# Optimization experiments

Measured on AMD Instinct MI355X. Metric: run time of the kernel, lower is better.

The kernel has to match this reference:

```python
import math
import jax, jax.numpy as jnp
import numpy as np

B = 2
TMAX = 1024
D = 1024
H = 16
DK = D // H
F = 4096
L = 2
CHUNK = 128
LEFT = 128
RIGHT = 32
EPS = 1e-5


def _build_mask(t_max, chunk, left, right):
    """Replicates EmformerEncoder.create_mask with audio_lens == t_max.
    Returns bool [T, T] where True = masked (disallowed), T = total_right + t_max."""
    num_chunks = math.ceil(t_max / chunk)
    ub = (num_chunks - 1) * right
    body = np.zeros((t_max, t_max), np.float32)
    mleft = np.zeros((t_max, ub), np.float32)
    mdiag = np.zeros((ub, ub), np.float32)
    mright = np.zeros((ub, t_max), np.float32)
    right_indexes = []
    for i in range(num_chunks):
        left_off = max(chunk * i - left, 0)
        start = chunk * i
        end = min(chunk * (i + 1), t_max)
        body[start:end, left_off:end] = 1
        if i == num_chunks - 1:
            break
        rem = t_max - (end + right)
        trl = right if rem >= 0 else t_max - end
        ri = len(right_indexes)
        mleft[start:start + chunk, ri:ri + trl] = 1
        mdiag[ri:ri + trl, ri:ri + trl] = 1
        mright[ri:ri + trl, left_off:end] = 1
        right_indexes += list(range(end, end + trl))
    rs = len(right_indexes)
    mleft = mleft[:, :rs]
    mdiag = mdiag[:rs, :rs]
    mright = mright[:rs, :]
    top = np.concatenate([mdiag, mright], axis=-1)
    bot = np.concatenate([mleft, body], axis=-1)
    m = np.concatenate([top, bot], axis=0)
    return m == 0  # True where attention is NOT allowed


def setup_inputs() -> dict:
    key = jax.random.key(0)
    ks = jax.random.split(key, 8)
    mask2d = _build_mask(TMAX, CHUNK, LEFT, RIGHT)  # [T, T]
    T = mask2d.shape[0]  # 1248
    w = lambda k, shape: jax.random.normal(k, shape, jnp.float32) * 0.02
    inp = {
        "input": jax.random.normal(ks[0], (B, T, D), jnp.float32),
        "ln_in_scale": jnp.ones((L, D), jnp.float32),
        "ln_in_bias": jnp.zeros((L, D), jnp.float32),
        "Wq": w(ks[1], (L, D, D)), "bq": jnp.zeros((L, D), jnp.float32),
        "Wk": w(ks[2], (L, D, D)), "bk": jnp.zeros((L, D), jnp.float32),
        "Wv": w(ks[3], (L, D, D)), "bv": jnp.zeros((L, D), jnp.float32),
        "ln1_scale": jnp.ones((L, D), jnp.float32),
        "ln1_bias": jnp.zeros((L, D), jnp.float32),
        "W1": w(ks[4], (L, D, F)), "b1": jnp.zeros((L, F), jnp.float32),
        "W2": w(ks[5], (L, F, D)), "b2": jnp.zeros((L, D), jnp.float32),
        "ln2_scale": jnp.ones((L, D), jnp.float32),
        "ln2_bias": jnp.zeros((L, D), jnp.float32),
        "mask": jnp.asarray(np.broadcast_to(mask2d[None, None], (B, 1, T, T)).copy()),
    }
    return inp


def _ln(x, scale, bias):
    m = jnp.mean(x, axis=-1, keepdims=True)
    v = jnp.mean(jnp.square(x - m), axis=-1, keepdims=True)
    return (x - m) * jax.lax.rsqrt(v + EPS) * scale + bias


def reference(input, ln_in_scale, ln_in_bias, Wq, bq, Wk, bk, Wv, bv,
              ln1_scale, ln1_bias, W1, b1, W2, b2, ln2_scale, ln2_bias, mask):
    x = input
    Bx, T, _ = x.shape
    scale = 1.0 / math.sqrt(DK)
    for l in range(L):
        h = _ln(x, ln_in_scale[l], ln_in_bias[l])  # pre-LN input (also residual base)
        q = (h @ Wq[l] + bq[l]).reshape(Bx, T, H, DK)
        k = (h @ Wk[l] + bk[l]).reshape(Bx, T, H, DK)
        v = (h @ Wv[l] + bv[l]).reshape(Bx, T, H, DK)
        scores = jnp.einsum('bqhd,bkhd->bhqk', q, k) * scale  # [B,H,T,T]
        scores = jnp.where(mask, -jnp.inf, scores)
        probs = jax.nn.softmax(scores, axis=-1)
        probs = jnp.where(mask, 0.0, probs)  # dropout_attn=0 -> identity
        o = jnp.einsum('bhqk,bkhd->bqhd', probs, v).reshape(Bx, T, D)
        attn_out = o + h
        y = _ln(attn_out, ln1_scale[l], ln1_bias[l])
        y = y @ W1[l] + b1[l]          # note: no activation in original code
        y = y @ W2[l] + b2[l] + attn_out
        x = _ln(y, ln2_scale[l], ln2_bias[l])
    return x
```

## Files before the change

### kernel.cpp

```cpp
#include <hip/hip_runtime.h>
#include <stdint.h>

typedef __attribute__((ext_vector_type(8))) short short8;
typedef __attribute__((ext_vector_type(4))) float f32x4;

#define DEV __device__ __forceinline__

DEV float bits2f(uint32_t u){ union{uint32_t u;float f;}v; v.u=u; return v.f; }
DEV float bf1(uint16_t s){ return bits2f(((uint32_t)s)<<16); }
DEV uint16_t f2bf(float f){ union{float f;uint32_t u;}v; v.f=f; uint32_t u=v.u;
  return (uint16_t)((u + 0x7fffu + ((u>>16)&1u))>>16); }
DEV uint16_t f2h(float a){ union{_Float16 h; uint16_t u;}v; v.h=(_Float16)a; return v.u; }
DEV float h2f(uint16_t s){ union{uint16_t u; _Float16 h;}v; v.u=s; return (float)v.h; }

DEV float ldval(const float* p, size_t i){ return p[i]; }
DEV float ldval(const uint16_t* p, size_t i){ return bf1(p[i]); }
DEV void stval(float* p, size_t i, float v){ p[i]=v; }
DEV void stval(uint16_t* p, size_t i, float v){ p[i]=f2bf(v); }

DEV void async16(const void* g, void* l){
#if __has_builtin(__builtin_amdgcn_global_load_lds)
  __builtin_amdgcn_global_load_lds((const __attribute__((address_space(1))) void*)g,
                                   (__attribute__((address_space(3))) void*)l, 16, 0, 0);
#else
  int lane = threadIdx.x & 63;
  *(uint4*)((char*)l + lane*16) = *(const uint4*)((const char*)g);
#endif
}

template<int TM, int TN, bool SPLIT>
__global__ __launch_bounds__(256) void gemm_t(
    const uint16_t* __restrict__ A, const uint16_t* __restrict__ Bt,
    const float* __restrict__ bias, void* __restrict__ Cout,
    int N, int K, int kchunk, ulong4 zofs) {
  __shared__ uint16_t sA[3][TM*32];
  __shared__ uint16_t sB[3][TN*32];
  constexpr int LPS = TM/64 + TN/64;
  const int lin = blockIdx.y*gridDim.x + blockIdx.x;
  const int q8 = (gridDim.x*gridDim.y) >> 3;
  const int swz = (lin & 7)*q8 + (lin >> 3);
  const int mt_ = swz % gridDim.y, nt_ = swz / gridDim.y;
  const int m0 = mt_*TM, n0 = nt_*TN;
  const int kb = SPLIT ? blockIdx.z*kchunk : 0;
  const int kend = SPLIT ? ((kb+kchunk < K) ? kb+kchunk : K) : K;
  const int tid = threadIdx.x, wid = tid>>6, lane = tid&63;
  constexpr int WM = TM/2, MT = WM/16;
  constexpr int WN = TN/2, NT = WN/16;
  const int wm = (wid&1)*WM, wn = (wid>>1)*WN;
  f32x4 acc[MT][NT];
  #pragma unroll
  for (int a=0;a<MT;a++)
    #pragma unroll
    for (int b=0;b<NT;b++) acc[a][b] = (f32x4){0.f,0.f,0.f,0.f};
  const int lrow = lane>>2;
  const int lcol = (((lane&3) ^ ((lrow>>1)&3)))*8;
  const int fr = lane&15, fc = lane>>4;
  const int rsw = (fc ^ ((fr>>1)&3))*8;

  auto stage = [&](int buf, int k0) {
    #pragma unroll
    for (int j = 0; j < TM/64; ++j) {
      int r0 = wid*(TM/4) + j*16;
      async16(A + (size_t)(m0+r0+lrow)*K + k0 + lcol, &sA[buf][r0*32]);
    }
    #pragma unroll
    for (int j = 0; j < TN/64; ++j) {
      int r0 = wid*(TN/4) + j*16;
      async16(Bt + (size_t)(n0+r0+lrow)*K + k0 + lcol, &sB[buf][r0*32]);
    }
  };

  const int niter = (kend - kb) >> 5;
  stage(0, kb);
  if (niter > 1) stage(1, kb + 32);
  int cur = 0;
  for (int it = 0; it < niter; ++it) {
    if (it+1 < niter) {
      if constexpr (LPS == 4)      asm volatile("s_waitcnt vmcnt(4)" ::: "memory");
      else if constexpr (LPS == 3) asm volatile("s_waitcnt vmcnt(3)" ::: "memory");
      else                         asm volatile("s_waitcnt vmcnt(2)" ::: "memory");
    } else {
      asm volatile("s_waitcnt vmcnt(0)" ::: "memory");
    }
    __builtin_amdgcn_s_barrier();
    __builtin_amdgcn_sched_barrier(0);
    if (it+2 < niter) {
      int b2 = cur+2; if (b2>=3) b2-=3;
      stage(b2, kb + (it+2)*32);
    }
    short8 af[MT], bfv[NT];
    #pragma unroll
    for (int t=0;t<MT;t++) af[t] = *(const short8*)&sA[cur][(wm + t*16 + fr)*32 + rsw];
    #pragma unroll
    for (int t=0;t<NT;t++) bfv[t] = *(const short8*)&sB[cur][(wn + t*16 + fr)*32 + rsw];
    #pragma unroll
    for (int mt=0;mt<MT;mt++)
      #pragma unroll
      for (int nt=0;nt<NT;nt++)
        acc[mt][nt] = __builtin_amdgcn_mfma_f32_16x16x32_bf16(af[mt], bfv[nt], acc[mt][nt], 0,0,0);
    if (++cur == 3) cur = 0;
  }
  const int cl = lane&15, rl = (lane>>4)*4;
  if (SPLIT) {
    size_t zo = (blockIdx.z==0) ? zofs.x : (blockIdx.z==1) ? zofs.y : zofs.z;
    float* Pz = (float*)((char*)Cout + zo);
    #pragma unroll
    for (int nt=0;nt<NT;nt++) {
      int n = n0 + wn + nt*16 + cl;
      #pragma unroll
      for (int mt=0;mt<MT;mt++)
        #pragma unroll
        for (int r=0;r<4;r++)
          Pz[(size_t)(m0 + wm + mt*16 + rl + r)*N + n] = acc[mt][nt][r];
    }
  } else {
    uint16_t* C = (uint16_t*)Cout;
    #pragma unroll
    for (int nt=0;nt<NT;nt++) {
      int n = n0 + wn + nt*16 + cl;
      float bv = bias ? bias[n] : 0.f;
      #pragma unroll
      for (int mt=0;mt<MT;mt++)
        #pragma unroll
        for (int r=0;r<4;r++)
          C[(size_t)(m0 + wm + mt*16 + rl + r)*N + n] = f2bf(acc[mt][nt][r] + bv);
    }
  }
}

template<typename TI, typename TO>
DEV void ln_body(int row, int tid, const TI* x, const float* sc, const float* bi,
                 TO* out, float* red) {
  const size_t base = (size_t)row*1024 + tid*4;
  float v0=ldval(x,base), v1=ldval(x,base+1), v2=ldval(x,base+2), v3=ldval(x,base+3);
  float s = v0+v1+v2+v3;
  float sq = v0*v0+v1*v1+v2*v2+v3*v3;
  #pragma unroll
  for (int off=32; off; off>>=1){ s += __shfl_xor(s,off); sq += __shfl_xor(sq,off); }
  int wid=tid>>6, lane=tid&63;
  if (lane==0){ red[wid]=s; red[4+wid]=sq; }
  __syncthreads();
  s = red[0]+red[1]+red[2]+red[3]; sq = red[4]+red[5]+red[6]+red[7];
  float mean = s*(1.f/1024.f);
  float inv  = rsqrtf(sq*(1.f/1024.f) - mean*mean + 1e-5f);
  int c = tid*4;
  stval(out, base,   (v0-mean)*inv*sc[c]   + bi[c]);
  stval(out, base+1, (v1-mean)*inv*sc[c+1] + bi[c+1]);
  stval(out, base+2, (v2-mean)*inv*sc[c+2] + bi[c+2]);
  stval(out, base+3, (v3-mean)*inv*sc[c+3] + bi[c+3]);
}

template<typename TI, typename TO>
__global__ __launch_bounds__(256) void ln_k(const TI* __restrict__ x,
    const float* __restrict__ sc, const float* __restrict__ bi,
    TO* __restrict__ out) {
  __shared__ float red[8];
  ln_body<TI,TO>(blockIdx.x, threadIdx.x, x, sc, bi, out, red);
}

template<typename TO>
__global__ __launch_bounds__(256) void ln2_fused(const char* __restrict__ wsb,
    const float* __restrict__ b2, const uint16_t* __restrict__ resid,
    const float* __restrict__ sc, const float* __restrict__ bi,
    TO* __restrict__ out) {
  const int row = blockIdx.x, tid = threadIdx.x;
  const size_t base = (size_t)row*1024 + tid*4;
  const float* P0 = (const float*)(wsb + 54538240);
  const float* P1 = (const float*)(wsb + 65024000);
  const float* P2 = (const float*)(wsb + 0);
  float4 p0 = *(const float4*)(P0 + base);
  float4 p1 = *(const float4*)(P1 + base);
  float4 p2 = *(const float4*)(P2 + base);
  int c = tid*4;
  float v0 = p0.x+p1.x+p2.x+b2[c]  +bf1(resid[base]);
  float v1 = p0.y+p1.y+p2.y+b2[c+1]+bf1(resid[base+1]);
  float v2 = p0.z+p1.z+p2.z+b2[c+2]+bf1(resid[base+2]);
  float v3 = p0.w+p1.w+p2.w+b2[c+3]+bf1(resid[base+3]);
  float s = v0+v1+v2+v3;
  float sq = v0*v0+v1*v1+v2*v2+v3*v3;
  #pragma unroll
  for (int off=32; off; off>>=1){ s += __shfl_xor(s,off); sq += __shfl_xor(sq,off); }
  __shared__ float red[8];
  int wid=tid>>6, lane=tid&63;
  if (lane==0){ red[wid]=s; red[4+wid]=sq; }
  __syncthreads();
  s = red[0]+red[1]+red[2]+red[3]; sq = red[4]+red[5]+red[6]+red[7];
  float mean = s*(1.f/1024.f);
  float inv  = rsqrtf(sq*(1.f/1024.f) - mean*mean + 1e-5f);
  stval(out, base,   (v0-mean)*inv*sc[c]   + bi[c]);
  stval(out, base+1, (v1-mean)*inv*sc[c+1] + bi[c+1]);
  stval(out, base+2, (v2-mean)*inv*sc[c+2] + bi[c+2]);
  stval(out, base+3, (v3-mean)*inv*sc[c+3] + bi[c+3]);
}

__global__ __launch_bounds__(256) void attn_fused(
    const uint32_t* __restrict__ qkv32, const uint16_t* __restrict__ hres,
    uint16_t* __restrict__ attn_out) {
  const int blk = blockIdx.x;
  const int qg = blk & 3, ci = (blk>>2)&7, hh = (blk>>5)&15, bb = blk>>9;
  const int sum_cnt = (ci<7)?32:0;
  const int bstart = (ci>=1)?128*(ci-1):0;
  const int bend = (ci==7)?1024:128*(ci+1);
  const int nk = sum_cnt + (bend - bstart);
  const int rowbase = bb*1248;
  const int tid = threadIdx.x, wid = tid>>6, lane = tid&63;
  const int fr = lane&15, fc = lane>>4;

  __shared__ __attribute__((aligned(16))) uint16_t sm[30848];
  uint16_t* K16 = sm;
  uint32_t* KD  = (uint32_t*)sm;
  uint16_t* Q16 = sm + 20736;
  uint32_t* QD  = KD + 10368;
  uint16_t* SP16 = sm;
  uint16_t* V16 = sm + 11840;
  uint32_t* VD  = (uint32_t*)(sm + 11840);

  for (int idx = tid; idx < nk*8; idx += 256) {
    int j = idx>>3, q4 = idx&7;
    int tk = (j < sum_cnt) ? (32*ci + j) : (224 + bstart + (j - sum_cnt));
    *(uint4*)&KD[j*36 + q4*4] =
      *(const uint4*)&qkv32[(size_t)(rowbase+tk)*1536 + 512 + hh*32 + q4*4];
  }
  for (int idx = tid; idx < 40*8; idx += 256) {
    int j = idx>>3, q4 = idx&7;
    int ql = qg*40 + j;
    int tq = (ql<32) ? (32*ci+ql) : (224+128*ci+ql-32);
    *(uint4*)&QD[j*36 + q4*4] =
      *(const uint4*)&qkv32[(size_t)(rowbase+tq)*1536 + hh*32 + q4*4];
  }
  __syncthreads();

  const int n_mt = nk>>4;
  const int qoff[3] = {0,16,24};
  f32x4 accs[5][3];
  #pragma unroll
  for (int a=0;a<5;a++)
    #pragma unroll
    for (int b=0;b<3;b++) accs[a][b] = (f32x4){0.f,0.f,0.f,0.f};
  __builtin_amdgcn_s_setprio(1);
  #pragma unroll
  for (int ks=0; ks<2; ++ks) {
    short8 bq_[3];
    #pragma unroll
    for (int nt=0;nt<3;nt++)
      bq_[nt] = *(const short8*)&Q16[(qoff[nt]+fr)*72 + ks*32 + fc*8];
    #pragma unroll
    for (int t=0;t<5;t++) {
      int mt = wid + 4*t;
      if (mt < n_mt) {
        short8 a_ = *(const short8*)&K16[(mt*16+fr)*72 + ks*32 + fc*8];
        #pragma unroll
        for (int nt=0;nt<3;nt++)
          accs[t][nt] = __builtin_amdgcn_mfma_f32_16x16x32_bf16(a_, bq_[nt], accs[t][nt], 0,0,0);
      }
    }
  }
  __builtin_amdgcn_s_setprio(0);
  __syncthreads();

  #pragma unroll
  for (int t=0;t<5;t++) {
    int mt = wid + 4*t;
    if (mt < n_mt) {
      #pragma unroll
      for (int nt=0;nt<3;nt++) {
        int q = qoff[nt] + fr;
        #pragma unroll
        for (int r=0;r<4;r++)
          SP16[q*296 + mt*16 + fc*4 + r] = f2h(accs[t][nt][r]*0.125f);
      }
    }
  }
  for (int idx = tid; idx < nk*8; idx += 256) {
    int j = idx>>3, q4 = idx&7;
    int tk = (j < sum_cnt) ? (32*ci + j) : (224 + bstart + (j - sum_cnt));
    uint4 w = *(const uint4*)&qkv32[(size_t)(rowbase+tk)*1536 + 1024 + hh*32 + q4*4];
    uint32_t* dst = &VD[j*33 + q4*4];
    dst[0]=w.x; dst[1]=w.y; dst[2]=w.z; dst[3]=w.w;
  }
  __syncthreads();

  for (int i=0;i<10;i++) {
    int row = wid*10 + i;
    float v[5];
    #pragma unroll
    for (int g=0;g<5;g++){ int k=g*64+lane; v[g] = (k<nk) ? h2f(SP16[row*296+k]) : -1e30f; }
    float mx = fmaxf(fmaxf(fmaxf(v[0],v[1]),fmaxf(v[2],v[3])),v[4]);
    #pragma unroll
    for (int off=32; off; off>>=1) mx = fmaxf(mx, __shfl_xor(mx,off));
    float p[5], sum=0.f;
    #pragma unroll
    for (int g=0;g<5;g++){ p[g] = __expf(v[g]-mx); if (g*64+lane>=nk) p[g]=0.f; sum+=p[g]; }
    #pragma unroll
    for (int off=32; off; off>>=1) sum += __shfl_xor(sum,off);
    float inv = 1.f/sum;
    #pragma unroll
    for (int g=0;g<5;g++){ int k=g*64+lane; if (k<nk) SP16[row*296+k] = f2bf(p[g]*inv); }
  }
  __syncthreads();

  const int nkt = nk>>5;
  f32x4 acco[3];
  #pragma unroll
  for (int t=0;t<3;t++) acco[t] = (f32x4){0.f,0.f,0.f,0.f};
  const uint16_t* vcol = V16 + wid*16 + fr;
  __builtin_amdgcn_s_setprio(1);
  for (int kt=0; kt<nkt; ++kt) {
    short8 bv_;
    #pragma unroll
    for (int j=0;j<8;j++) bv_[j] = (short)vcol[(kt*32 + fc*8 + j)*66];
    #pragma unroll
    for (int t=0;t<3;t++) {
      short8 a_ = *(const short8*)&SP16[(qoff[t]+fr)*296 + kt*32 + fc*8];
      acco[t] = __builtin_amdgcn_mfma_f32_16x16x32_bf16(a_, bv_, acco[t], 0,0,0);
    }
  }
  __builtin_amdgcn_s_setprio(0);
  #pragma unroll
  for (int t=0;t<3;t++) {
    #pragma unroll
    for (int r=0;r<4;r++) {
      bool vq = true;
      if (ci==7 && qg==0 && (qoff[t]+fc*4+r)<32) vq = false;
      if (vq) {
        int qll = qg*40 + qoff[t] + fc*4 + r;
        int tq = (qll<32) ? (32*ci+qll) : (224+128*ci+qll-32);
        size_t addr = (size_t)(rowbase+tq)*1024 + hh*64 + wid*16 + fr;
        attn_out[addr] = f2bf(acco[t][r] + bf1(hres[addr]));
      }
    }
  }
}

__global__ void prep_k(const float* __restrict__ Wq, const float* __restrict__ Wk,
                       const float* __restrict__ Wv, const float* __restrict__ W1,
                       const float* __restrict__ W2, const float* __restrict__ bq,
                       const float* __restrict__ bk, const float* __restrict__ bv,
                       uint16_t* __restrict__ wt_qkv, uint16_t* __restrict__ wt_w1,
                       uint16_t* __restrict__ wt_w2, float* __restrict__ bqkv,
                       const void* __restrict__ lnx, int lnx_f32,
                       const float* __restrict__ lnsc, const float* __restrict__ lnbi,
                       uint16_t* __restrict__ lnout) {
  __shared__ float t[32][33];
  const int blk = blockIdx.x;
  const int tx = threadIdx.x, ty = threadIdx.y;
  if (blk >= 11276) {
    int row = blk - 11276;
    int tid = ty*32 + tx;
    float* red = &t[0][0];
    if (lnx_f32) ln_body<float,uint16_t>((int)row, tid, (const float*)lnx, lnsc, lnbi, lnout, red);
    else         ln_body<uint16_t,uint16_t>((int)row, tid, (const uint16_t*)lnx, lnsc, lnbi, lnout, red);
    return;
  }
  if (blk >= 11264) {
    int i = (blk-11264)*256 + ty*32 + tx;
    bqkv[i] = (i<1024) ? bq[i] : ((i<2048) ? bk[i-1024] : bv[i-2048]);
    return;
  }
  const float* src; uint16_t* dst; int R, C, c0, r0;
  if (blk < 3072) {
    int w = blk>>10, tt = blk&1023;
    src = (w==0)?Wq:((w==1)?Wk:Wv); dst = wt_qkv + (size_t)w*1048576;
    R = 1024; C = 1024; c0 = (tt&31)*32; r0 = (tt>>5)*32;
  } else if (blk < 7168) {
    int tt = blk-3072;
    src = W1; dst = wt_w1; R = 1024; C = 4096;
    c0 = (tt&127)*32; r0 = (tt>>7)*32;
  } else {
    int tt = blk-7168;
    src = W2; dst = wt_w2; R = 4096; C = 1024;
    c0 = (tt&31)*32; r0 = (tt>>5)*32;
  }
  #pragma unroll
  for (int i=0;i<4;i++) t[ty+8*i][tx] = src[(size_t)(r0+ty+8*i)*C + c0+tx];
  __syncthreads();
  #pragma unroll
  for (int i=0;i<4;i++) dst[(size_t)(c0+ty+8*i)*R + r0+tx] = f2bf(t[tx][ty+8*i]);
}

extern "C" void kernel_launch(void* const* d_in, const int* in_sizes, int n_in,
                              void* d_out, int out_size, void* d_ws, size_t ws_size,
                              hipStream_t stream) {
  const float* input  = (const float*)d_in[0];
  const float* lnin_s = (const float*)d_in[1];
  const float* lnin_b = (const float*)d_in[2];
  const float* Wq = (const float*)d_in[3];
  const float* bq = (const float*)d_in[4];
  const float* Wk = (const float*)d_in[5];
  const float* bk = (const float*)d_in[6];
  const float* Wv = (const float*)d_in[7];
  const float* bv = (const float*)d_in[8];
  const float* ln1_s = (const float*)d_in[9];
  const float* ln1_b = (const float*)d_in[10];
  const float* W1 = (const float*)d_in[11];
  const float* b1 = (const float*)d_in[12];
  const float* W2 = (const float*)d_in[13];
  const float* b2 = (const float*)d_in[14];
  const float* ln2_s = (const float*)d_in[15];
  const float* ln2_b = (const float*)d_in[16];

  char* ws = (char*)d_ws;
  uint16_t* wt_qkv = (uint16_t*)(ws + 0);
  uint16_t* wt_w1  = (uint16_t*)(ws + 6291456);
  uint16_t* wt_w2  = (uint16_t*)(ws + 14680064);
  float*    bqkv   = (float*)   (ws + 23068672);
  uint16_t* hbuf   = (uint16_t*)(ws + 23080960);
  uint16_t* qkvb   = (uint16_t*)(ws + 28323840);
  uint16_t* attnb  = (uint16_t*)(ws + 44052480);
  uint16_t* zbuf   = (uint16_t*)(ws + 49295360);
  uint16_t* y1b    = hbuf;
  uint16_t* x1b    = zbuf;

  const ulong4 zofs{54538240ull, 65024000ull, 0ull, 0ull};
  const ulong4 z0{0ull,0ull,0ull,0ull};

  const uint16_t* xcur_bf = x1b;
  for (int l=0; l<2; ++l) {
    prep_k<<<13772, dim3(32,8), 0, stream>>>(Wq+(size_t)l*1048576, Wk+(size_t)l*1048576,
        Wv+(size_t)l*1048576, W1+(size_t)l*4194304, W2+(size_t)l*4194304,
        bq+l*1024, bk+l*1024, bv+l*1024, wt_qkv, wt_w1, wt_w2, bqkv,
        (l==0) ? (const void*)input : (const void*)xcur_bf, (l==0)?1:0,
        lnin_s+l*1024, lnin_b+l*1024, hbuf);

    gemm_t<128,64,false><<<dim3(48,20),256,0,stream>>>(hbuf, wt_qkv, bqkv, qkvb, 3072, 1024, 1024, z0);
    attn_fused<<<1024,256,0,stream>>>((const uint32_t*)qkvb, hbuf, attnb);
    ln_k<uint16_t,uint16_t><<<2496,256,0,stream>>>(attnb, ln1_s+l*1024, ln1_b+l*1024, zbuf);
    gemm_t<128,64,false><<<dim3(64,20),256,0,stream>>>(zbuf, wt_w1, b1+l*4096, y1b, 4096, 1024, 1024, z0);
    gemm_t<128,64,true><<<dim3(16,20,3),256,0,stream>>>(y1b, wt_w2, nullptr, ws, 1024, 4096, 1376, zofs);
    if (l==1) ln2_fused<float>   <<<2496,256,0,stream>>>(ws, b2+l*1024, attnb, ln2_s+l*1024, ln2_b+l*1024, (float*)d_out);
    else      ln2_fused<uint16_t><<<2496,256,0,stream>>>(ws, b2+l*1024, attnb, ln2_s+l*1024, ln2_b+l*1024, x1b);
  }
  (void)in_sizes; (void)n_in; (void)out_size; (void)ws_size;
}
```

Before: 514.7 us.

## Replace GEMM with 256x256-tile 8-wave kernel using double-buffered K=64 stages

Replaces the 128x64 tile, 4-wave, triple-buffered GEMM with a 256x256 tile, 8-wave (512-thread) kernel. It stages K=64 slices into double-buffered LDS with an XOR swizzle and raises wave priority around the MFMA blocks. The grid swizzle is dropped and the split-K chunk for W2 changes to 1408. Larger tiles give more data reuse per LDS load, but the grids shrink to 120-160 blocks on a 256-CU part (W2: 120 blocks), which risks underfilling the device. Each block also holds 128 KB of LDS.

```diff
diff --git a/kernel.cpp b/kernel.cpp
--- a/kernel.cpp
+++ b/kernel.cpp
@@ -28,87 +28,74 @@
 #endif
 }
 
-template<int TM, int TN, bool SPLIT>
-__global__ __launch_bounds__(256) void gemm_t(
+template<bool SPLIT>
+__global__ __launch_bounds__(512, 2) void gemm8(
     const uint16_t* __restrict__ A, const uint16_t* __restrict__ Bt,
     const float* __restrict__ bias, void* __restrict__ Cout,
     int N, int K, int kchunk, ulong4 zofs) {
-  __shared__ uint16_t sA[3][TM*32];
-  __shared__ uint16_t sB[3][TN*32];
-  constexpr int LPS = TM/64 + TN/64;
-  const int lin = blockIdx.y*gridDim.x + blockIdx.x;
-  const int q8 = (gridDim.x*gridDim.y) >> 3;
-  const int swz = (lin & 7)*q8 + (lin >> 3);
-  const int mt_ = swz % gridDim.y, nt_ = swz / gridDim.y;
-  const int m0 = mt_*TM, n0 = nt_*TN;
+  __shared__ uint16_t sA[2][256*64];
+  __shared__ uint16_t sB[2][256*64];
+  const int m0 = blockIdx.y*256, n0 = blockIdx.x*256;
   const int kb = SPLIT ? blockIdx.z*kchunk : 0;
   const int kend = SPLIT ? ((kb+kchunk < K) ? kb+kchunk : K) : K;
   const int tid = threadIdx.x, wid = tid>>6, lane = tid&63;
-  constexpr int WM = TM/2, MT = WM/16;
-  constexpr int WN = TN/2, NT = WN/16;
-  const int wm = (wid&1)*WM, wn = (wid>>1)*WN;
-  f32x4 acc[MT][NT];
-  #pragma unroll
-  for (int a=0;a<MT;a++)
-    #pragma unroll
-    for (int b=0;b<NT;b++) acc[a][b] = (f32x4){0.f,0.f,0.f,0.f};
-  const int lrow = lane>>2;
-  const int lcol = (((lane&3) ^ ((lrow>>1)&3)))*8;
   const int fr = lane&15, fc = lane>>4;
-  const int rsw = (fc ^ ((fr>>1)&3))*8;
+  const int wm = (wid&1)*128, wn = (wid>>1)*64;
+  const int srow = lane>>3;
+  const int gsw  = ((lane&7) ^ srow)*8;
+
+  f32x4 acc[8][4];
+  #pragma unroll
+  for (int a=0;a<8;a++)
+    #pragma unroll
+    for (int b=0;b<4;b++) acc[a][b] = (f32x4){0.f,0.f,0.f,0.f};
 
   auto stage = [&](int buf, int k0) {
     #pragma unroll
-    for (int j = 0; j < TM/64; ++j) {
-      int r0 = wid*(TM/4) + j*16;
-      async16(A + (size_t)(m0+r0+lrow)*K + k0 + lcol, &sA[buf][r0*32]);
-    }
-    #pragma unroll
-    for (int j = 0; j < TN/64; ++j) {
-      int r0 = wid*(TN/4) + j*16;
-      async16(Bt + (size_t)(n0+r0+lrow)*K + k0 + lcol, &sB[buf][r0*32]);
+    for (int j=0;j<4;++j) {
+      const int r0 = wid*8 + j*64;
+      async16(A + (size_t)(m0+r0+srow)*K + k0 + gsw, &sA[buf][r0*64]);
+      async16(Bt + (size_t)(n0+r0+srow)*K + k0 + gsw, &sB[buf][r0*64]);
     }
   };
 
-  const int niter = (kend - kb) >> 5;
+  const int niter = (kend - kb) >> 6;
   stage(0, kb);
-  if (niter > 1) stage(1, kb + 32);
+  asm volatile("s_waitcnt vmcnt(0)" ::: "memory");
+  __builtin_amdgcn_s_barrier();
   int cur = 0;
   for (int it = 0; it < niter; ++it) {
-    if (it+1 < niter) {
-      if constexpr (LPS == 4)      asm volatile("s_waitcnt vmcnt(4)" ::: "memory");
-      else if constexpr (LPS == 3) asm volatile("s_waitcnt vmcnt(3)" ::: "memory");
-      else                         asm volatile("s_waitcnt vmcnt(2)" ::: "memory");
-    } else {
-      asm volatile("s_waitcnt vmcnt(0)" ::: "memory");
-    }
+    if (it+1 < niter) stage(cur^1, kb + (it+1)*64);
+    #pragma unroll
+    for (int ks=0; ks<2; ++ks) {
+      const int sl = ((ks*4 + fc) ^ (fr&7))*8;
+      short8 af[8], bfv[4];
+      #pragma unroll
+      for (int mt=0;mt<8;mt++) af[mt] = *(const short8*)&sA[cur][(wm+mt*16+fr)*64 + sl];
+      #pragma unroll
+      for (int nt=0;nt<4;nt++) bfv[nt] = *(const short8*)&sB[cur][(wn+nt*16+fr)*64 + sl];
+      __builtin_amdgcn_s_setprio(1);
+      #pragma unroll
+      for (int mt=0;mt<8;mt++)
+        #pragma unroll
+        for (int nt=0;nt<4;nt++)
+          acc[mt][nt] = __builtin_amdgcn_mfma_f32_16x16x32_bf16(af[mt], bfv[nt], acc[mt][nt], 0,0,0);
+      __builtin_amdgcn_s_setprio(0);
+    }
+    asm volatile("s_waitcnt vmcnt(0)" ::: "memory");
     __builtin_amdgcn_s_barrier();
-    __builtin_amdgcn_sched_barrier(0);
-    if (it+2 < niter) {
-      int b2 = cur+2; if (b2>=3) b2-=3;
-      stage(b2, kb + (it+2)*32);
-    }
-    short8 af[MT], bfv[NT];
-    #pragma unroll
-    for (int t=0;t<MT;t++) af[t] = *(const short8*)&sA[cur][(wm + t*16 + fr)*32 + rsw];
-    #pragma unroll
-    for (int t=0;t<NT;t++) bfv[t] = *(const short8*)&sB[cur][(wn + t*16 + fr)*32 + rsw];
-    #pragma unroll
-    for (int mt=0;mt<MT;mt++)
-      #pragma unroll
-      for (int nt=0;nt<NT;nt++)
-        acc[mt][nt] = __builtin_amdgcn_mfma_f32_16x16x32_bf16(af[mt], bfv[nt], acc[mt][nt], 0,0,0);
-    if (++cur == 3) cur = 0;
-  }
+    cur ^= 1;
+  }
+
   const int cl = lane&15, rl = (lane>>4)*4;
   if (SPLIT) {
     size_t zo = (blockIdx.z==0) ? zofs.x : (blockIdx.z==1) ? zofs.y : zofs.z;
     float* Pz = (float*)((char*)Cout + zo);
     #pragma unroll
-    for (int nt=0;nt<NT;nt++) {
+    for (int nt=0;nt<4;nt++) {
       int n = n0 + wn + nt*16 + cl;
       #pragma unroll
-      for (int mt=0;mt<MT;mt++)
+      for (int mt=0;mt<8;mt++)
         #pragma unroll
         for (int r=0;r<4;r++)
           Pz[(size_t)(m0 + wm + mt*16 + rl + r)*N + n] = acc[mt][nt][r];
@@ -116,11 +103,11 @@
   } else {
     uint16_t* C = (uint16_t*)Cout;
     #pragma unroll
-    for (int nt=0;nt<NT;nt++) {
+    for (int nt=0;nt<4;nt++) {
       int n = n0 + wn + nt*16 + cl;
       float bv = bias ? bias[n] : 0.f;
       #pragma unroll
-      for (int mt=0;mt<MT;mt++)
+      for (int mt=0;mt<8;mt++)
         #pragma unroll
         for (int r=0;r<4;r++)
           C[(size_t)(m0 + wm + mt*16 + rl + r)*N + n] = f2bf(acc[mt][nt][r] + bv);
@@ -422,11 +409,11 @@
         (l==0) ? (const void*)input : (const void*)xcur_bf, (l==0)?1:0,
         lnin_s+l*1024, lnin_b+l*1024, hbuf);
 
-    gemm_t<128,64,false><<<dim3(48,20),256,0,stream>>>(hbuf, wt_qkv, bqkv, qkvb, 3072, 1024, 1024, z0);
+    gemm8<false><<<dim3(12,10),512,0,stream>>>(hbuf, wt_qkv, bqkv, qkvb, 3072, 1024, 0, z0);
     attn_fused<<<1024,256,0,stream>>>((const uint32_t*)qkvb, hbuf, attnb);
     ln_k<uint16_t,uint16_t><<<2496,256,0,stream>>>(attnb, ln1_s+l*1024, ln1_b+l*1024, zbuf);
-    gemm_t<128,64,false><<<dim3(64,20),256,0,stream>>>(zbuf, wt_w1, b1+l*4096, y1b, 4096, 1024, 1024, z0);
-    gemm_t<128,64,true><<<dim3(16,20,3),256,0,stream>>>(y1b, wt_w2, nullptr, ws, 1024, 4096, 1376, zofs);
+    gemm8<false><<<dim3(16,10),512,0,stream>>>(zbuf, wt_w1, b1+l*4096, y1b, 4096, 1024, 0, z0);
+    gemm8<true><<<dim3(4,10,3),512,0,stream>>>(y1b, wt_w2, nullptr, ws, 1024, 4096, 1408, zofs);
     if (l==1) ln2_fused<float>   <<<2496,256,0,stream>>>(ws, b2+l*1024, attnb, ln2_s+l*1024, ln2_b+l*1024, (float*)d_out);
     else      ln2_fused<uint16_t><<<2496,256,0,stream>>>(ws, b2+l*1024, attnb, ln2_s+l*1024, ln2_b+l*1024, x1b);
   }
```

Measured after the change: 529.8 us. 2.9% more time.
